# Kernel tuning notes

Hardware: AMD Instinct MI355X
Metric: run time of the kernel (lower is better)

## Reference

```python
import jax, jax.numpy as jnp
import numpy as np


def setup_inputs() -> dict:
    key = jax.random.key(0)
    k0, k1, k2, k3 = jax.random.split(key, 4)
    B, M, H, K, OUT = 256, 64, 64, 128, 256
    x0 = jax.random.normal(k0, (B, M, K), dtype=jnp.float32)
    xl = jax.random.normal(k1, (B, H, K), dtype=jnp.float32)
    # Conv1d(in_channels=M*H, out_channels=OUT, kernel_size=1) params
    fan_in = M * H  # kernel_size=1
    bound = 1.0 / np.sqrt(fan_in)
    W = jax.random.uniform(k2, (OUT, M * H, 1), dtype=jnp.float32, minval=-bound, maxval=bound)
    b = jax.random.uniform(k3, (OUT,), dtype=jnp.float32, minval=-bound, maxval=bound)
    return {"x0": x0, "xl": xl, "k": K, "W": W, "b": b}


def reference(x0, xl, k, W, b):
    # x0: [B, m, k_emb], xl: [B, h, k_emb]
    # Fused equivalent of the per-column loop: for each embedding column i,
    # matmul(xl[:,:,i:i+1], x0[:,:,i:i+1]^T) -> [B,h,m]; stacked over k -> [B,h,m,k]
    fmap = jnp.einsum('bhk,bmk->bhmk', xl, x0)
    B = x0.shape[0]
    h, m = xl.shape[1], x0.shape[1]
    fmap = fmap.reshape(B, h * m, k)  # [B, h*m, k]
    # 1x1 Conv1d == GEMM over channel dim
    out = jnp.einsum('bck,oc->bok', fmap, W[:, :, 0]) + b[None, :, None]
    return out
```

## Files before the change

kernel.cpp:

```cpp
#include <hip/hip_runtime.h>
#include <hip/hip_bf16.h>
#include <stdint.h>


typedef __attribute__((ext_vector_type(8))) short short8;
typedef __attribute__((ext_vector_type(4))) float f32x4;

#define B_SZ   256
#define K_SZ   128
#define OUT_SZ 256
#define C_SZ   4096
#define NCHUNK 64

__device__ __forceinline__ uint32_t pack_bf16(float a, float b) {
    __hip_bfloat162 h2 = __float22bfloat162_rn(make_float2(a, b));
    union { __hip_bfloat162 h; uint32_t u; } v;
    v.h = h2;
    return v.u;
}

__device__ __forceinline__ void load_lds_16(const void* g, void* l) {
    __builtin_amdgcn_global_load_lds(
        (const __attribute__((address_space(1))) unsigned int*)g,
        (__attribute__((address_space(3))) unsigned int*)l,
        16, 0, 0);
}

__global__ void convert_W_tiled(const float* __restrict__ W, short* __restrict__ Wb) {
    int t = blockIdx.x * blockDim.x + threadIdx.x;
    int lane = t & 63;
    int cb   = (t >> 6) & 127;
    int got  = t >> 13;
    int o = got * 16 + (lane & 15);
    int c = cb * 32 + (lane >> 4) * 8;
    const float* p = W + (size_t)o * C_SZ + c;
    float4 w0 = *(const float4*)p;
    float4 w1 = *(const float4*)(p + 4);
    union { short8 s; uint32_t u[4]; } cc;
    cc.u[0] = pack_bf16(w0.x, w0.y);
    cc.u[1] = pack_bf16(w0.z, w0.w);
    cc.u[2] = pack_bf16(w1.x, w1.y);
    cc.u[3] = pack_bf16(w1.z, w1.w);
    *(short8*)(Wb + (size_t)t * 8) = cc.s;
}

template<bool USE_WS>
__global__ __launch_bounds__(512, 4)
void cin_main(const float* __restrict__ x0, const float* __restrict__ xl,
              const float* __restrict__ Wf, const short* __restrict__ Wb,
              const float* __restrict__ bias, float* __restrict__ out) {
    __shared__ float xlf[64 * 128];
    __shared__ short Wlds[2 * 8192];

    const int b     = blockIdx.y;
    const int ohalf = blockIdx.x;
    const int tid   = threadIdx.x;
    const int lane  = tid & 63;
    const int wave  = tid >> 6;
    const int wk    = wave & 3;
    const int wo    = wave >> 2;
    const int rl    = lane & 15;
    const int kg    = lane >> 4;

    {
        const float4* src = (const float4*)(xl + (size_t)b * (64 * K_SZ));
        float4* dst = (float4*)xlf;
#pragma unroll
        for (int i = 0; i < 4; ++i)
            dst[tid * 4 + i] = src[tid * 4 + i];
    }

    float x0f[2][2][8];
    {
        const float* x0b = x0 + (size_t)b * (64 * K_SZ);
        const int col0 = wk * 32 + rl;
#pragma unroll
        for (int mi = 0; mi < 2; ++mi)
#pragma unroll
            for (int j = 0; j < 8; ++j) {
                const float* r = x0b + (mi * 32 + kg * 8 + j) * K_SZ + col0;
                x0f[mi][0][j] = r[0];
                x0f[mi][1][j] = r[16];
            }
    }

    const short* wsrc = Wb + ((size_t)(ohalf * 8 + wave) * 128) * 512 + lane * 8;
    const float* wfrow = Wf + (size_t)((ohalf * 8 + wave) * 16 + rl) * C_SZ + kg * 8;
    short* wdst0 = Wlds + (wave * 2 + 0) * 512;
    short* wdst1 = Wlds + (wave * 2 + 1) * 512;
    short* wown  = Wlds + (wave * 2) * 512 + lane * 8;

    auto stage = [&](int buf, int h) {
        if (USE_WS) {
            const short* s = wsrc + (size_t)h * 1024;
            load_lds_16(s,       wdst0 + buf * 8192);
            load_lds_16(s + 512, wdst1 + buf * 8192);
        } else {
#pragma unroll
            for (int cbl = 0; cbl < 2; ++cbl) {
                const float* p = wfrow + (2 * h + cbl) * 32;
                float4 w0 = *(const float4*)p;
                float4 w1 = *(const float4*)(p + 4);
                union { short8 s; uint32_t u[4]; } cc;
                cc.u[0] = pack_bf16(w0.x, w0.y);
                cc.u[1] = pack_bf16(w0.z, w0.w);
                cc.u[2] = pack_bf16(w1.x, w1.y);
                cc.u[3] = pack_bf16(w1.z, w1.w);
                *(short8*)(wown + buf * 8192 + cbl * 512) = cc.s;
            }
        }
    };

    f32x4 acc[4][2];
#pragma unroll
    for (int ot = 0; ot < 4; ++ot)
#pragma unroll
        for (int nt = 0; nt < 2; ++nt)
            acc[ot][nt] = (f32x4){0.f, 0.f, 0.f, 0.f};

    stage(0, 0);
    __syncthreads();

    const float* xlrow = xlf + wk * 32 + rl;
    int cur = 0;

    for (int h = 0; h < NCHUNK; ++h) {
        if (h < NCHUNK - 1) stage(cur ^ 1, h + 1);

        const float xlv0 = xlrow[h * K_SZ];
        const float xlv1 = xlrow[h * K_SZ + 16];

#pragma unroll
        for (int mi = 0; mi < 2; ++mi) {
            const short* wbase = Wlds + cur * 8192 + (wo * 8 + mi) * 512 + lane * 8;

            union { short8 s; uint32_t u[4]; } bf0, bf1;
#pragma unroll
            for (int jj = 0; jj < 4; ++jj) {
                bf0.u[jj] = pack_bf16(xlv0 * x0f[mi][0][2 * jj], xlv0 * x0f[mi][0][2 * jj + 1]);
                bf1.u[jj] = pack_bf16(xlv1 * x0f[mi][1][2 * jj], xlv1 * x0f[mi][1][2 * jj + 1]);
            }

#pragma unroll
            for (int ot = 0; ot < 4; ++ot) {
                const short8 af = *(const short8*)(wbase + ot * 1024);
                acc[ot][0] = __builtin_amdgcn_mfma_f32_16x16x32_bf16(af, bf0.s, acc[ot][0], 0, 0, 0);
                acc[ot][1] = __builtin_amdgcn_mfma_f32_16x16x32_bf16(af, bf1.s, acc[ot][1], 0, 0, 0);
            }
        }
        __syncthreads();
        cur ^= 1;
    }

    const int obase = ohalf * 128 + wo * 64;
    const int kcol0 = wk * 32 + rl;
    float* outb = out + (size_t)b * (OUT_SZ * K_SZ);
#pragma unroll
    for (int ot = 0; ot < 4; ++ot) {
        const int o0 = obase + ot * 16 + kg * 4;
#pragma unroll
        for (int r = 0; r < 4; ++r) {
            const float bv = bias[o0 + r];
            outb[(o0 + r) * K_SZ + kcol0]      = acc[ot][0][r] + bv;
            outb[(o0 + r) * K_SZ + kcol0 + 16] = acc[ot][1][r] + bv;
        }
    }
}

extern "C" void kernel_launch(void* const* d_in, const int* in_sizes, int n_in,
                              void* d_out, int out_size, void* d_ws, size_t ws_size,
                              hipStream_t stream) {
    const float* x0   = (const float*)d_in[0];
    const float* xl   = (const float*)d_in[1];
    const float* W    = (const float*)d_in[3];
    const float* bias = (const float*)d_in[4];
    float* out = (float*)d_out;

    const size_t w_bytes = (size_t)OUT_SZ * C_SZ * sizeof(short);
    short* Wb = (short*)d_ws;

    if (ws_size >= w_bytes) {
        convert_W_tiled<<<dim3(512), dim3(256), 0, stream>>>(W, Wb);
        cin_main<true><<<dim3(2, B_SZ), dim3(512), 0, stream>>>(x0, xl, W, Wb, bias, out);
    } else {
        cin_main<false><<<dim3(2, B_SZ), dim3(512), 0, stream>>>(x0, xl, W, Wb, bias, out);
    }
}
```

Baseline: 88.12 us.

## Factor xl scaling out of MFMA operands, contracting W against bf16 x0 per h

The bilinear product is reordered so each h-chunk's MFMAs contract W against a bf16 x0 fragment that is packed once before the loop. Each partial result is then scaled by the fp32 xl value and accumulated with VALU FMAs. This removes the per-iteration multiply-and-pack of xl*x0 into bf16 B operands. The wave-to-tile mapping changes to 4 output groups by 2 k-halves. The cost is extra fp32 FMAs per iteration and a dependent two-MFMA chain per tile whose result must be read back before the FMAs, which may expose MFMA latency.

New measurement: 77.57 us. 1.14x faster.

```diff
diff --git a/kernel.cpp b/kernel.cpp
--- a/kernel.cpp
+++ b/kernel.cpp
@@ -57,8 +57,8 @@
     const int tid   = threadIdx.x;
     const int lane  = tid & 63;
     const int wave  = tid >> 6;
-    const int wk    = wave & 3;
-    const int wo    = wave >> 2;
+    const int wo    = wave >> 1;
+    const int wk    = wave & 1;
     const int rl    = lane & 15;
     const int kg    = lane >> 4;
 
@@ -70,18 +70,21 @@
             dst[tid * 4 + i] = src[tid * 4 + i];
     }
 
-    float x0f[2][2][8];
+    union { short8 s; uint32_t u[4]; } x0p[2][4];
     {
         const float* x0b = x0 + (size_t)b * (64 * K_SZ);
-        const int col0 = wk * 32 + rl;
+        const int col0 = wk * 64 + rl;
 #pragma unroll
-        for (int mi = 0; mi < 2; ++mi)
+        for (int ks = 0; ks < 2; ++ks)
 #pragma unroll
-            for (int j = 0; j < 8; ++j) {
-                const float* r = x0b + (mi * 32 + kg * 8 + j) * K_SZ + col0;
-                x0f[mi][0][j] = r[0];
-                x0f[mi][1][j] = r[16];
-            }
+            for (int nt = 0; nt < 4; ++nt)
+#pragma unroll
+                for (int j = 0; j < 4; ++j) {
+                    const int r0 = ks * 32 + kg * 8 + 2 * j;
+                    const int cc = col0 + nt * 16;
+                    x0p[ks][nt].u[j] = pack_bf16(x0b[r0 * K_SZ + cc],
+                                                 x0b[(r0 + 1) * K_SZ + cc]);
+                }
     }
 
     const short* wsrc = Wb + ((size_t)(ohalf * 8 + wave) * 128) * 512 + lane * 8;
@@ -111,58 +114,56 @@
         }
     };
 
-    f32x4 acc[4][2];
+    f32x4 acc[2][4];
 #pragma unroll
-    for (int ot = 0; ot < 4; ++ot)
+    for (int ot = 0; ot < 2; ++ot)
 #pragma unroll
-        for (int nt = 0; nt < 2; ++nt)
+        for (int nt = 0; nt < 4; ++nt)
             acc[ot][nt] = (f32x4){0.f, 0.f, 0.f, 0.f};
+    const f32x4 kz = (f32x4){0.f, 0.f, 0.f, 0.f};
 
     stage(0, 0);
     __syncthreads();
 
-    const float* xlrow = xlf + wk * 32 + rl;
+    const float* xlrow = xlf + wk * 64 + rl;
     int cur = 0;
 
     for (int h = 0; h < NCHUNK; ++h) {
         if (h < NCHUNK - 1) stage(cur ^ 1, h + 1);
 
-        const float xlv0 = xlrow[h * K_SZ];
-        const float xlv1 = xlrow[h * K_SZ + 16];
+        float xlv[4];
+#pragma unroll
+        for (int nt = 0; nt < 4; ++nt)
+            xlv[nt] = xlrow[h * K_SZ + nt * 16];
 
 #pragma unroll
-        for (int mi = 0; mi < 2; ++mi) {
-            const short* wbase = Wlds + cur * 8192 + (wo * 8 + mi) * 512 + lane * 8;
-
-            union { short8 s; uint32_t u[4]; } bf0, bf1;
+        for (int ot = 0; ot < 2; ++ot) {
+            const short* wb = Wlds + cur * 8192 + ((wo * 2 + ot) * 2) * 512 + lane * 8;
+            const short8 af0 = *(const short8*)(wb);
+            const short8 af1 = *(const short8*)(wb + 512);
 #pragma unroll
-            for (int jj = 0; jj < 4; ++jj) {
-                bf0.u[jj] = pack_bf16(xlv0 * x0f[mi][0][2 * jj], xlv0 * x0f[mi][0][2 * jj + 1]);
-                bf1.u[jj] = pack_bf16(xlv1 * x0f[mi][1][2 * jj], xlv1 * x0f[mi][1][2 * jj + 1]);
-            }
-
+            for (int nt = 0; nt < 4; ++nt) {
+                f32x4 g = __builtin_amdgcn_mfma_f32_16x16x32_bf16(af0, x0p[0][nt].s, kz, 0, 0, 0);
+                g = __builtin_amdgcn_mfma_f32_16x16x32_bf16(af1, x0p[1][nt].s, g, 0, 0, 0);
 #pragma unroll
-            for (int ot = 0; ot < 4; ++ot) {
-                const short8 af = *(const short8*)(wbase + ot * 1024);
-                acc[ot][0] = __builtin_amdgcn_mfma_f32_16x16x32_bf16(af, bf0.s, acc[ot][0], 0, 0, 0);
-                acc[ot][1] = __builtin_amdgcn_mfma_f32_16x16x32_bf16(af, bf1.s, acc[ot][1], 0, 0, 0);
+                for (int r = 0; r < 4; ++r)
+                    acc[ot][nt][r] += xlv[nt] * g[r];
             }
         }
         __syncthreads();
         cur ^= 1;
     }
 
-    const int obase = ohalf * 128 + wo * 64;
-    const int kcol0 = wk * 32 + rl;
     float* outb = out + (size_t)b * (OUT_SZ * K_SZ);
 #pragma unroll
-    for (int ot = 0; ot < 4; ++ot) {
-        const int o0 = obase + ot * 16 + kg * 4;
+    for (int ot = 0; ot < 2; ++ot) {
+        const int o0 = ohalf * 128 + wo * 32 + ot * 16 + kg * 4;
 #pragma unroll
         for (int r = 0; r < 4; ++r) {
             const float bv = bias[o0 + r];
-            outb[(o0 + r) * K_SZ + kcol0]      = acc[ot][0][r] + bv;
-            outb[(o0 + r) * K_SZ + kcol0 + 16] = acc[ot][1][r] + bv;
+#pragma unroll
+            for (int nt = 0; nt < 4; ++nt)
+                outb[(o0 + r) * K_SZ + wk * 64 + nt * 16 + rl] = acc[ot][nt][r] + bv;
         }
     }
 }
```
